# Kernel tuning notes

Measured on AMD Instinct MI355X. Metric: run time of the kernel, lower is better.

Reference implementation:

```python
import jax, jax.numpy as jnp
import numpy as np

N_ATOMS = 100000
N_EDGES = 800000
ATOM_DIM = 32
BOND_DIM = 16


def setup_inputs() -> dict:
    key = jax.random.key(0)
    k1, k2, k3, k4 = jax.random.split(key, 4)
    atom_features = jax.random.normal(k1, (N_ATOMS, ATOM_DIM), dtype=jnp.float32)
    bond_features = jax.random.normal(k2, (N_EDGES, BOND_DIM), dtype=jnp.float32)
    pair_indices = jax.random.randint(k3, (N_EDGES, 2), 0, N_ATOMS, dtype=jnp.int64 if jax.config.jax_enable_x64 else jnp.int32)
    # glorot-uniform-ish kernel
    limit = np.sqrt(6.0 / (BOND_DIM + ATOM_DIM * ATOM_DIM))
    kernel = jax.random.uniform(k4, (BOND_DIM, ATOM_DIM * ATOM_DIM), dtype=jnp.float32, minval=-limit, maxval=limit)
    bias = jnp.zeros((ATOM_DIM * ATOM_DIM,), dtype=jnp.float32)
    return {"atom_features": atom_features, "bond_features": bond_features,
            "pair_indices": pair_indices, "kernel": kernel, "bias": bias}


def reference(atom_features, bond_features, pair_indices, kernel, bias):
    atom_dim = atom_features.shape[-1]
    n_atoms = atom_features.shape[0]
    # bond-conditioned per-edge transform matrices: [E, atom_dim, atom_dim]
    bt = (bond_features @ kernel + bias).reshape(-1, atom_dim, atom_dim)
    # gather neighbor atom features: [E, atom_dim]
    neigh = atom_features[pair_indices[:, 1]]
    # per-edge small matmul: messages [E, atom_dim]
    messages = jnp.einsum('eij,ej->ei', bt, neigh)
    # scatter-add to destination atoms
    aggregated = jax.ops.segment_sum(messages, pair_indices[:, 0], num_segments=n_atoms)
    return aggregated
```

## Files before the change

### kernel.cpp

```cpp
#include <hip/hip_runtime.h>
#include <hip/hip_bf16.h>

typedef __attribute__((ext_vector_type(8))) short short8;
typedef __attribute__((ext_vector_type(4))) short s16x4;
typedef __attribute__((ext_vector_type(4))) float f32x4;

#define N_ATOMS 100000
#define N_EDGES 800000
#define N_TILES (N_EDGES/16)
#define WAVE_PAIRS 2048
#define N_CHUNKS ((N_ATOMS + 255) / 256)

#define WS_MSG     0ULL
#define WS_OFFS    51200000ULL
#define WS_COUNTS  51600016ULL
#define WS_EDATA   52000016ULL
#define WS_RANK    58400016ULL
#define WS_PART    61600016ULL
#define WS_NEED    61602064ULL

__device__ __forceinline__ short f2bf(float x) {
    __hip_bfloat16 h = __float2bfloat16(x);
    return __builtin_bit_cast(short, h);
}
__device__ __forceinline__ float bf2f(short b) {
    unsigned u = ((unsigned)(unsigned short)b) << 16;
    return __builtin_bit_cast(float, u);
}

__global__ __launch_bounds__(256) void zero_ints(int* __restrict__ p, int n) {
    int i = blockIdx.x * 256 + threadIdx.x;
    if (i < n) p[i] = 0;
}

__global__ __launch_bounds__(256) void rank_kernel(const int2* __restrict__ pair,
                                                   int* __restrict__ counts,
                                                   int* __restrict__ rank) {
    int e = blockIdx.x * 256 + threadIdx.x;
    if (e < N_EDGES) rank[e] = atomicAdd(&counts[pair[e].x], 1);
}

__global__ __launch_bounds__(256) void scan_part(const int* __restrict__ counts,
                                                 int* __restrict__ partials) {
    const int tid = threadIdx.x;
    const int i = blockIdx.x * 256 + tid;
    int v = (i < N_ATOMS) ? counts[i] : 0;
#pragma unroll
    for (int off = 1; off < 64; off <<= 1) v += __shfl_xor(v, off);
    __shared__ int ws4[4];
    const int lane = tid & 63, wv = tid >> 6;
    if (lane == 0) ws4[wv] = v;
    __syncthreads();
    if (tid == 0) partials[blockIdx.x] = ws4[0] + ws4[1] + ws4[2] + ws4[3];
}

__global__ __launch_bounds__(512) void scan_mid(int* __restrict__ partials) {
    const int tid = threadIdx.x;
    const int lane = tid & 63, wv = tid >> 6;
    int v = (tid < N_CHUNKS) ? partials[tid] : 0;
    int inc = v;
#pragma unroll
    for (int off = 1; off < 64; off <<= 1) {
        int u = __shfl_up(inc, off);
        if (lane >= off) inc += u;
    }
    __shared__ int ws8[8];
    if (lane == 63) ws8[wv] = inc;
    __syncthreads();
    int base = 0;
#pragma unroll
    for (int k = 0; k < 8; ++k) base += (k < wv) ? ws8[k] : 0;
    if (tid < N_CHUNKS) partials[tid] = base + inc - v;
}

__global__ __launch_bounds__(256) void scan_final(const int* __restrict__ counts,
                                                  const int* __restrict__ partials,
                                                  int* __restrict__ offsets) {
    const int tid = threadIdx.x;
    const int i = blockIdx.x * 256 + tid;
    const int lane = tid & 63, wv = tid >> 6;
    int c = (i < N_ATOMS) ? counts[i] : 0;
    int inc = c;
#pragma unroll
    for (int off = 1; off < 64; off <<= 1) {
        int u = __shfl_up(inc, off);
        if (lane >= off) inc += u;
    }
    __shared__ int ws4[4];
    if (lane == 63) ws4[wv] = inc;
    __syncthreads();
    int base = partials[blockIdx.x];
#pragma unroll
    for (int k = 0; k < 4; ++k) base += (k < wv) ? ws4[k] : 0;
    const int off = base + inc - c;
    if (i < N_ATOMS) offsets[i] = off;
    if (i == N_ATOMS - 1) offsets[N_ATOMS] = off + c;
}

__global__ __launch_bounds__(256) void edata_kernel(const int2* __restrict__ pair,
                                                    const int* __restrict__ offsets,
                                                    const int* __restrict__ rank,
                                                    int2* __restrict__ edata) {
    int e = blockIdx.x * 256 + threadIdx.x;
    if (e < N_EDGES) {
        int2 p = pair[e];
        int2 d;
        d.x = p.y;
        d.y = offsets[p.x] + rank[e];
        edata[e] = d;
    }
}

__global__ __launch_bounds__(256, 3)
void edge_msg_kernel(const float* __restrict__ atom,
                     const float* __restrict__ bond,
                     const float* __restrict__ kern,
                     const float* __restrict__ bias,
                     const int2*  __restrict__ edata,
                     short*       __restrict__ msg)
{
    __shared__ __align__(16) char smem[32768];
    short* klds = (short*)smem;
    float* blds = (float*)smem;

    const int tid = threadIdx.x;
    for (int x = tid; x < 16*2*512; x += 256) {
        const int t = x & 7;
        const int l = (x >> 3) & 63;
        const int m = (x >> 9) & 1;
        const int b = x >> 10;
        const int i = m*16 + (l & 15);
        const int j = ((l >> 4) << 3) + t;
        klds[x] = f2bf(kern[b*1024 + i*32 + j]);
    }
    __syncthreads();

    const int wave = tid >> 6;
    const int lane = tid & 63;
    const int er   = lane & 15;
    const int jg   = lane >> 4;
    const int wid  = blockIdx.x * 4 + wave;
    const int m    = wid & 1;
    const int pid  = wid >> 1;

    short8 afr[16];
#pragma unroll
    for (int b = 0; b < 16; ++b)
        afr[b] = *(const short8*)&klds[(b*2 + m)*512 + lane*8];

    short8 af16;
    {
        const float* bp = bias + (m*16 + er)*32 + jg*8;
        const f32x4 z0 = *(const f32x4*)bp;
        const f32x4 z1 = *(const f32x4*)(bp + 4);
        af16[0]=f2bf(z0[0]); af16[1]=f2bf(z0[1]); af16[2]=f2bf(z0[2]); af16[3]=f2bf(z0[3]);
        af16[4]=f2bf(z1[0]); af16[5]=f2bf(z1[1]); af16[6]=f2bf(z1[2]); af16[7]=f2bf(z1[3]);
    }
    __syncthreads();

    const int ibase = m*16 + jg*4;

    float* bwA = blds + (0*4 + wave)*320 + (lane >> 2)*20 + (lane & 3)*4;
    float* bwB = blds + (1*4 + wave)*320 + (lane >> 2)*20 + (lane & 3)*4;
    const float* brA = blds + (0*4 + wave)*320 + er*20;
    const float* brB = blds + (1*4 + wave)*320 + er*20;

    const int last = N_TILES - 1;

    const int tA = pid;
    const int tB = (pid + WAVE_PAIRS <= last) ? pid + WAVE_PAIRS : last;
    int2  e0 = edata[tA*16 + er];
    f32x4 bv0 = *(const f32x4*)(bond + tA*256 + lane*4);
    int2  e1 = edata[tB*16 + er];
    f32x4 bv1 = *(const f32x4*)(bond + tB*256 + lane*4);
    f32x4 n0 = *(const f32x4*)(atom + e0.x*32 + jg*8);
    f32x4 n1 = *(const f32x4*)(atom + e0.x*32 + jg*8 + 4);
    *(f32x4*)bwA = bv0;

    for (int t = pid; t < N_TILES; t += WAVE_PAIRS) {
        int tn2 = t + 2*WAVE_PAIRS; tn2 = (tn2 <= last) ? tn2 : last;
        const int2  e2  = edata[tn2*16 + er];
        const f32x4 bv2 = *(const f32x4*)(bond + tn2*256 + lane*4);

        const f32x4 n0n = *(const f32x4*)(atom + e1.x*32 + jg*8);
        const f32x4 n1n = *(const f32x4*)(atom + e1.x*32 + jg*8 + 4);

        const f32x4 q0 = *(const f32x4*)(brA + 0);
        const f32x4 q1 = *(const f32x4*)(brA + 4);
        const f32x4 q2 = *(const f32x4*)(brA + 8);
        const f32x4 q3 = *(const f32x4*)(brA + 12);

        short8 bfrag;
        bfrag[0] = f2bf(n0[0]); bfrag[1] = f2bf(n0[1]);
        bfrag[2] = f2bf(n0[2]); bfrag[3] = f2bf(n0[3]);
        bfrag[4] = f2bf(n1[0]); bfrag[5] = f2bf(n1[1]);
        bfrag[6] = f2bf(n1[2]); bfrag[7] = f2bf(n1[3]);

        float bb[16];
        bb[0]=q0[0];  bb[1]=q0[1];  bb[2]=q0[2];  bb[3]=q0[3];
        bb[4]=q1[0];  bb[5]=q1[1];  bb[6]=q1[2];  bb[7]=q1[3];
        bb[8]=q2[0];  bb[9]=q2[1];  bb[10]=q2[2]; bb[11]=q2[3];
        bb[12]=q3[0]; bb[13]=q3[1]; bb[14]=q3[2]; bb[15]=q3[3];

        f32x4 macc = {0.f,0.f,0.f,0.f};
        const f32x4 z = {0.f,0.f,0.f,0.f};
#pragma unroll
        for (int b = 0; b < 16; ++b) {
            f32x4 d = __builtin_amdgcn_mfma_f32_16x16x32_bf16(afr[b], bfrag, z, 0, 0, 0);
            macc[0] = fmaf(bb[b], d[0], macc[0]);
            macc[1] = fmaf(bb[b], d[1], macc[1]);
            macc[2] = fmaf(bb[b], d[2], macc[2]);
            macc[3] = fmaf(bb[b], d[3], macc[3]);
        }
        {
            f32x4 d = __builtin_amdgcn_mfma_f32_16x16x32_bf16(af16, bfrag, z, 0, 0, 0);
            macc[0] += d[0]; macc[1] += d[1]; macc[2] += d[2]; macc[3] += d[3];
        }

        *(f32x4*)bwB = bv1;

        s16x4 mv;
        mv[0] = f2bf(macc[0]); mv[1] = f2bf(macc[1]);
        mv[2] = f2bf(macc[2]); mv[3] = f2bf(macc[3]);
        *(s16x4*)&msg[(long long)e0.y*32 + ibase] = mv;

        e0 = e1; e1 = e2; bv1 = bv2; n0 = n0n; n1 = n1n;
        float* tw = bwA; bwA = bwB; bwB = tw;
        const float* tr = brA; brA = brB; brB = tr;
    }
}

__global__ __launch_bounds__(256) void gather_kernel(const short* __restrict__ msg,
                                                     const int* __restrict__ offsets,
                                                     float* __restrict__ out) {
    const int tid = threadIdx.x;
    const int a = blockIdx.x * 32 + (tid >> 3);
    const int sub = (tid & 7) * 4;
    if (a >= N_ATOMS) return;
    const int b0 = offsets[a], b1 = offsets[a + 1];
    f32x4 acc0 = {0.f, 0.f, 0.f, 0.f};
    f32x4 acc1 = {0.f, 0.f, 0.f, 0.f};
    int k = b0;
    for (; k + 1 < b1; k += 2) {
        s16x4 mv0 = *(const s16x4*)&msg[k*32 + sub];
        s16x4 mv1 = *(const s16x4*)&msg[(k+1)*32 + sub];
        acc0[0] += bf2f(mv0[0]); acc0[1] += bf2f(mv0[1]);
        acc0[2] += bf2f(mv0[2]); acc0[3] += bf2f(mv0[3]);
        acc1[0] += bf2f(mv1[0]); acc1[1] += bf2f(mv1[1]);
        acc1[2] += bf2f(mv1[2]); acc1[3] += bf2f(mv1[3]);
    }
    if (k < b1) {
        s16x4 mv0 = *(const s16x4*)&msg[k*32 + sub];
        acc0[0] += bf2f(mv0[0]); acc0[1] += bf2f(mv0[1]);
        acc0[2] += bf2f(mv0[2]); acc0[3] += bf2f(mv0[3]);
    }
    acc0[0] += acc1[0]; acc0[1] += acc1[1]; acc0[2] += acc1[2]; acc0[3] += acc1[3];
    *(f32x4*)&out[a*32 + sub] = acc0;
}

__global__ __launch_bounds__(256) void zero_out(f32x4* __restrict__ out) {
    int i = blockIdx.x * 256 + threadIdx.x;
    f32x4 z = {0.f, 0.f, 0.f, 0.f};
    out[i] = z;
}

__global__ __launch_bounds__(256, 4)
void edge_kernel_atomic(const float* __restrict__ atom, const float* __restrict__ bond,
                        const int2* __restrict__ pair, const float* __restrict__ kern,
                        const float* __restrict__ bias, float* __restrict__ out)
{
    __shared__ __align__(16) short alds[17*2*512];
    const int tid = threadIdx.x;
    for (int x = tid; x < 17*2*512; x += 256) {
        const int t = x & 7;
        const int l = (x >> 3) & 63;
        const int m = (x >> 9) & 1;
        const int b = x >> 10;
        const int i = m*16 + (l & 15);
        const int j = ((l >> 4) << 3) + t;
        const float v = (b < 16) ? kern[b*1024 + i*32 + j] : bias[i*32 + j];
        alds[x] = f2bf(v);
    }
    __syncthreads();
    const int wave = tid >> 6, lane = tid & 63;
    const int er = lane & 15, jg = lane >> 4;
    const int wid = blockIdx.x * 4 + wave;
    const int m = wid & 1, pid = wid >> 1;
    short8 afr[17];
#pragma unroll
    for (int b = 0; b < 17; ++b)
        afr[b] = *(const short8*)&alds[(b*2 + m)*512 + lane*8];
    const int ibase = m*16 + jg*4;
    for (int tile = pid; tile < N_TILES; tile += WAVE_PAIRS) {
        const int e = tile*16 + er;
        const int2 p = pair[e];
        const f32x4* arow = (const f32x4*)(atom + p.y * 32);
        const f32x4 n0 = arow[jg*2];
        const f32x4 n1 = arow[jg*2 + 1];
        short8 bfrag;
        bfrag[0] = f2bf(n0[0]); bfrag[1] = f2bf(n0[1]);
        bfrag[2] = f2bf(n0[2]); bfrag[3] = f2bf(n0[3]);
        bfrag[4] = f2bf(n1[0]); bfrag[5] = f2bf(n1[1]);
        bfrag[6] = f2bf(n1[2]); bfrag[7] = f2bf(n1[3]);
        const f32x4* brow = (const f32x4*)(bond + e * 16);
        const f32x4 q0 = brow[0], q1 = brow[1], q2 = brow[2], q3 = brow[3];
        float bb[17];
        bb[0]=q0[0];  bb[1]=q0[1];  bb[2]=q0[2];  bb[3]=q0[3];
        bb[4]=q1[0];  bb[5]=q1[1];  bb[6]=q1[2];  bb[7]=q1[3];
        bb[8]=q2[0];  bb[9]=q2[1];  bb[10]=q2[2]; bb[11]=q2[3];
        bb[12]=q3[0]; bb[13]=q3[1]; bb[14]=q3[2]; bb[15]=q3[3];
        bb[16]=1.0f;
        f32x4 macc = {0.f,0.f,0.f,0.f};
#pragma unroll
        for (int b = 0; b < 17; ++b) {
            f32x4 z = {0.f,0.f,0.f,0.f};
            f32x4 d = __builtin_amdgcn_mfma_f32_16x16x32_bf16(afr[b], bfrag, z, 0, 0, 0);
            macc[0] = fmaf(bb[b], d[0], macc[0]);
            macc[1] = fmaf(bb[b], d[1], macc[1]);
            macc[2] = fmaf(bb[b], d[2], macc[2]);
            macc[3] = fmaf(bb[b], d[3], macc[3]);
        }
        float* obase = out + p.x * 32 + ibase;
        atomicAdd(obase + 0, macc[0]);
        atomicAdd(obase + 1, macc[1]);
        atomicAdd(obase + 2, macc[2]);
        atomicAdd(obase + 3, macc[3]);
    }
}

extern "C" void kernel_launch(void* const* d_in, const int* in_sizes, int n_in,
                              void* d_out, int out_size, void* d_ws, size_t ws_size,
                              hipStream_t stream)
{
    (void)in_sizes; (void)n_in; (void)out_size;
    const float* atom = (const float*)d_in[0];
    const float* bond = (const float*)d_in[1];
    const int2*  pair = (const int2*)d_in[2];
    const float* kern = (const float*)d_in[3];
    const float* bias = (const float*)d_in[4];
    float* out = (float*)d_out;

    if (ws_size < WS_NEED) {
        zero_out<<<dim3(N_ATOMS*32/4/256), dim3(256), 0, stream>>>((f32x4*)out);
        edge_kernel_atomic<<<dim3(1024), dim3(256), 0, stream>>>(atom, bond, pair, kern, bias, out);
        return;
    }

    char* ws = (char*)d_ws;
    short* msg    = (short*)(ws + WS_MSG);
    int* offsets  = (int*)(ws + WS_OFFS);
    int* counts   = (int*)(ws + WS_COUNTS);
    int2* edata   = (int2*)(ws + WS_EDATA);
    int* rank     = (int*)(ws + WS_RANK);
    int* partials = (int*)(ws + WS_PART);

    const int eb = (N_EDGES + 255) / 256;
    zero_ints<<<dim3((N_ATOMS + 255)/256), dim3(256), 0, stream>>>(counts, N_ATOMS);
    rank_kernel<<<dim3(eb), dim3(256), 0, stream>>>(pair, counts, rank);
    scan_part<<<dim3(N_CHUNKS), dim3(256), 0, stream>>>(counts, partials);
    scan_mid<<<dim3(1), dim3(512), 0, stream>>>(partials);
    scan_final<<<dim3(N_CHUNKS), dim3(256), 0, stream>>>(counts, partials, offsets);
    edata_kernel<<<dim3(eb), dim3(256), 0, stream>>>(pair, offsets, rank, edata);
    edge_msg_kernel<<<dim3(1024), dim3(256), 0, stream>>>(atom, bond, kern, bias, edata, msg);
    gather_kernel<<<dim3((N_ATOMS + 31)/32), dim3(256), 0, stream>>>(msg, offsets, out);
}
```

Before: 117.2 us.

## Deepen edge-message prefetch pipeline and replace LDS bond staging with shuffles

Restructures the edge message kernel. The grid now has 1250 blocks, so each wave pair handles exactly 20 tiles, and the loop is a fixed 5x4 unrolled sequence. Edge data and bond rows are prefetched four tiles ahead and atom rows two tiles ahead, which raises the number of memory requests in flight. Bond values are now spread across lanes with wave shuffles instead of being staged through a double-buffered LDS area, which removes the LDS writes, reads and one barrier but adds 16 shuffles per tile and more live registers. The tile counts are hardcoded, so the kernel depends on N_TILES being exactly 20×2500.

```diff
diff --git a/kernel.cpp b/kernel.cpp
--- a/kernel.cpp
+++ b/kernel.cpp
@@ -8,8 +8,10 @@
 #define N_ATOMS 100000
 #define N_EDGES 800000
 #define N_TILES (N_EDGES/16)
-#define WAVE_PAIRS 2048
 #define N_CHUNKS ((N_ATOMS + 255) / 256)
+
+#define MSG_BLOCKS 1250
+#define S_TILES    2500
 
 #define WS_MSG     0ULL
 #define WS_OFFS    51200000ULL
@@ -119,9 +121,7 @@
                      const int2*  __restrict__ edata,
                      short*       __restrict__ msg)
 {
-    __shared__ __align__(16) char smem[32768];
-    short* klds = (short*)smem;
-    float* blds = (float*)smem;
+    __shared__ __align__(16) short klds[16*2*512];
 
     const int tid = threadIdx.x;
     for (int x = tid; x < 16*2*512; x += 256) {
@@ -156,78 +156,74 @@
         af16[0]=f2bf(z0[0]); af16[1]=f2bf(z0[1]); af16[2]=f2bf(z0[2]); af16[3]=f2bf(z0[3]);
         af16[4]=f2bf(z1[0]); af16[5]=f2bf(z1[1]); af16[6]=f2bf(z1[2]); af16[7]=f2bf(z1[3]);
     }
-    __syncthreads();
 
     const int ibase = m*16 + jg*4;
-
-    float* bwA = blds + (0*4 + wave)*320 + (lane >> 2)*20 + (lane & 3)*4;
-    float* bwB = blds + (1*4 + wave)*320 + (lane >> 2)*20 + (lane & 3)*4;
-    const float* brA = blds + (0*4 + wave)*320 + er*20;
-    const float* brB = blds + (1*4 + wave)*320 + er*20;
-
-    const int last = N_TILES - 1;
+    const int last  = N_TILES - 1;
 
     const int tA = pid;
-    const int tB = (pid + WAVE_PAIRS <= last) ? pid + WAVE_PAIRS : last;
-    int2  e0 = edata[tA*16 + er];
-    f32x4 bv0 = *(const f32x4*)(bond + tA*256 + lane*4);
-    int2  e1 = edata[tB*16 + er];
-    f32x4 bv1 = *(const f32x4*)(bond + tB*256 + lane*4);
-    f32x4 n0 = *(const f32x4*)(atom + e0.x*32 + jg*8);
-    f32x4 n1 = *(const f32x4*)(atom + e0.x*32 + jg*8 + 4);
-    *(f32x4*)bwA = bv0;
-
-    for (int t = pid; t < N_TILES; t += WAVE_PAIRS) {
-        int tn2 = t + 2*WAVE_PAIRS; tn2 = (tn2 <= last) ? tn2 : last;
-        const int2  e2  = edata[tn2*16 + er];
-        const f32x4 bv2 = *(const f32x4*)(bond + tn2*256 + lane*4);
-
-        const f32x4 n0n = *(const f32x4*)(atom + e1.x*32 + jg*8);
-        const f32x4 n1n = *(const f32x4*)(atom + e1.x*32 + jg*8 + 4);
-
-        const f32x4 q0 = *(const f32x4*)(brA + 0);
-        const f32x4 q1 = *(const f32x4*)(brA + 4);
-        const f32x4 q2 = *(const f32x4*)(brA + 8);
-        const f32x4 q3 = *(const f32x4*)(brA + 12);
-
-        short8 bfrag;
-        bfrag[0] = f2bf(n0[0]); bfrag[1] = f2bf(n0[1]);
-        bfrag[2] = f2bf(n0[2]); bfrag[3] = f2bf(n0[3]);
-        bfrag[4] = f2bf(n1[0]); bfrag[5] = f2bf(n1[1]);
-        bfrag[6] = f2bf(n1[2]); bfrag[7] = f2bf(n1[3]);
-
-        float bb[16];
-        bb[0]=q0[0];  bb[1]=q0[1];  bb[2]=q0[2];  bb[3]=q0[3];
-        bb[4]=q1[0];  bb[5]=q1[1];  bb[6]=q1[2];  bb[7]=q1[3];
-        bb[8]=q2[0];  bb[9]=q2[1];  bb[10]=q2[2]; bb[11]=q2[3];
-        bb[12]=q3[0]; bb[13]=q3[1]; bb[14]=q3[2]; bb[15]=q3[3];
-
-        f32x4 macc = {0.f,0.f,0.f,0.f};
-        const f32x4 z = {0.f,0.f,0.f,0.f};
-#pragma unroll
-        for (int b = 0; b < 16; ++b) {
-            f32x4 d = __builtin_amdgcn_mfma_f32_16x16x32_bf16(afr[b], bfrag, z, 0, 0, 0);
-            macc[0] = fmaf(bb[b], d[0], macc[0]);
-            macc[1] = fmaf(bb[b], d[1], macc[1]);
-            macc[2] = fmaf(bb[b], d[2], macc[2]);
-            macc[3] = fmaf(bb[b], d[3], macc[3]);
-        }
-        {
-            f32x4 d = __builtin_amdgcn_mfma_f32_16x16x32_bf16(af16, bfrag, z, 0, 0, 0);
-            macc[0] += d[0]; macc[1] += d[1]; macc[2] += d[2]; macc[3] += d[3];
-        }
-
-        *(f32x4*)bwB = bv1;
-
-        s16x4 mv;
-        mv[0] = f2bf(macc[0]); mv[1] = f2bf(macc[1]);
-        mv[2] = f2bf(macc[2]); mv[3] = f2bf(macc[3]);
-        *(s16x4*)&msg[(long long)e0.y*32 + ibase] = mv;
-
-        e0 = e1; e1 = e2; bv1 = bv2; n0 = n0n; n1 = n1n;
-        float* tw = bwA; bwA = bwB; bwB = tw;
-        const float* tr = brA; brA = brB; brB = tr;
-    }
+    const int tB = min(pid + 1*S_TILES, last);
+    const int tC = min(pid + 2*S_TILES, last);
+    const int tD = min(pid + 3*S_TILES, last);
+    int2  eA = edata[tA*16 + er];  f32x4 bvA = *(const f32x4*)(bond + tA*256 + lane*4);
+    int2  eB = edata[tB*16 + er];  f32x4 bvB = *(const f32x4*)(bond + tB*256 + lane*4);
+    int2  eC = edata[tC*16 + er];  f32x4 bvC = *(const f32x4*)(bond + tC*256 + lane*4);
+    int2  eD = edata[tD*16 + er];  f32x4 bvD = *(const f32x4*)(bond + tD*256 + lane*4);
+    f32x4 n0P = *(const f32x4*)(atom + eA.x*32 + jg*8);
+    f32x4 n1P = *(const f32x4*)(atom + eA.x*32 + jg*8 + 4);
+    f32x4 n0Q = *(const f32x4*)(atom + eB.x*32 + jg*8);
+    f32x4 n1Q = *(const f32x4*)(atom + eB.x*32 + jg*8 + 4);
+
+#define EMK_BODY(EC, BVC, N0, N1, EG, TK)                                          \
+    {                                                                              \
+        float bb[16];                                                              \
+        _Pragma("unroll")                                                          \
+        for (int q = 0; q < 4; ++q) {                                              \
+            const int sl2 = (er << 2) | q;                                         \
+            bb[q*4+0] = __shfl(BVC[0], sl2);                                       \
+            bb[q*4+1] = __shfl(BVC[1], sl2);                                       \
+            bb[q*4+2] = __shfl(BVC[2], sl2);                                       \
+            bb[q*4+3] = __shfl(BVC[3], sl2);                                       \
+        }                                                                          \
+        const int sl = EC.y;                                                       \
+        short8 bfrag;                                                              \
+        bfrag[0]=f2bf(N0[0]); bfrag[1]=f2bf(N0[1]);                                \
+        bfrag[2]=f2bf(N0[2]); bfrag[3]=f2bf(N0[3]);                                \
+        bfrag[4]=f2bf(N1[0]); bfrag[5]=f2bf(N1[1]);                                \
+        bfrag[6]=f2bf(N1[2]); bfrag[7]=f2bf(N1[3]);                                \
+        const int t4 = min((TK) + 4*S_TILES, last);                                \
+        EC  = edata[t4*16 + er];                                                   \
+        BVC = *(const f32x4*)(bond + t4*256 + lane*4);                             \
+        N0  = *(const f32x4*)(atom + EG.x*32 + jg*8);                              \
+        N1  = *(const f32x4*)(atom + EG.x*32 + jg*8 + 4);                          \
+        f32x4 macc = {0.f,0.f,0.f,0.f};                                            \
+        const f32x4 z = {0.f,0.f,0.f,0.f};                                         \
+        _Pragma("unroll")                                                          \
+        for (int b = 0; b < 16; ++b) {                                             \
+            f32x4 d = __builtin_amdgcn_mfma_f32_16x16x32_bf16(afr[b], bfrag, z, 0, 0, 0); \
+            macc[0] = fmaf(bb[b], d[0], macc[0]);                                  \
+            macc[1] = fmaf(bb[b], d[1], macc[1]);                                  \
+            macc[2] = fmaf(bb[b], d[2], macc[2]);                                  \
+            macc[3] = fmaf(bb[b], d[3], macc[3]);                                  \
+        }                                                                          \
+        {                                                                          \
+            f32x4 d = __builtin_amdgcn_mfma_f32_16x16x32_bf16(af16, bfrag, z, 0, 0, 0); \
+            macc[0] += d[0]; macc[1] += d[1]; macc[2] += d[2]; macc[3] += d[3];    \
+        }                                                                          \
+        s16x4 mv;                                                                  \
+        mv[0]=f2bf(macc[0]); mv[1]=f2bf(macc[1]);                                  \
+        mv[2]=f2bf(macc[2]); mv[3]=f2bf(macc[3]);                                  \
+        *(s16x4*)&msg[sl*32 + ibase] = mv;                                         \
+    }
+
+#pragma unroll 1
+    for (int o = 0; o < 5; ++o) {
+        const int tb = pid + o*4*S_TILES;
+        EMK_BODY(eA, bvA, n0P, n1P, eC, tb + 0*S_TILES);
+        EMK_BODY(eB, bvB, n0Q, n1Q, eD, tb + 1*S_TILES);
+        EMK_BODY(eC, bvC, n0P, n1P, eA, tb + 2*S_TILES);
+        EMK_BODY(eD, bvD, n0Q, n1Q, eB, tb + 3*S_TILES);
+    }
+#undef EMK_BODY
 }
 
 __global__ __launch_bounds__(256) void gather_kernel(const short* __restrict__ msg,
@@ -291,7 +287,7 @@
     for (int b = 0; b < 17; ++b)
         afr[b] = *(const short8*)&alds[(b*2 + m)*512 + lane*8];
     const int ibase = m*16 + jg*4;
-    for (int tile = pid; tile < N_TILES; tile += WAVE_PAIRS) {
+    for (int tile = pid; tile < N_TILES; tile += 2048) {
         const int e = tile*16 + er;
         const int2 p = pair[e];
         const f32x4* arow = (const f32x4*)(atom + p.y * 32);
@@ -361,6 +357,6 @@
     scan_mid<<<dim3(1), dim3(512), 0, stream>>>(partials);
     scan_final<<<dim3(N_CHUNKS), dim3(256), 0, stream>>>(counts, partials, offsets);
     edata_kernel<<<dim3(eb), dim3(256), 0, stream>>>(pair, offsets, rank, edata);
-    edge_msg_kernel<<<dim3(1024), dim3(256), 0, stream>>>(atom, bond, kern, bias, edata, msg);
+    edge_msg_kernel<<<dim3(MSG_BLOCKS), dim3(256), 0, stream>>>(atom, bond, kern, bias, edata, msg);
     gather_kernel<<<dim3((N_ATOMS + 31)/32), dim3(256), 0, stream>>>(msg, offsets, out);
 }
```

New measurement: 127.3 us. 1.09x slower.

## Compute both output halves per wave to halve redundant edge gathers

Applied to the files above, without the earlier changes.

Each wave now handles all 32 output rows of a 16-edge tile instead of splitting them across a wave pair. The goal is to load the neighbor atom rows, bond features and edge data once per tile rather than twice. One half of the kernel fragments stays in registers and the other half, plus the bias, is read from LDS every iteration; an empty asm offset stops the compiler from hoisting those LDS loads into registers. The bond staging buffer becomes single-buffered per wave, and the grid shrinks to 768 blocks. The trade-off is more LDS traffic and longer per-wave dependency chains in place of duplicated global loads.

```diff
diff --git a/kernel.cpp b/kernel.cpp
--- a/kernel.cpp
+++ b/kernel.cpp
@@ -8,8 +8,10 @@
 #define N_ATOMS 100000
 #define N_EDGES 800000
 #define N_TILES (N_EDGES/16)
-#define WAVE_PAIRS 2048
 #define N_CHUNKS ((N_ATOMS + 255) / 256)
+
+#define MSG_BLOCKS 768
+#define MSG_WAVES  (MSG_BLOCKS*4)
 
 #define WS_MSG     0ULL
 #define WS_OFFS    51200000ULL
@@ -119,19 +121,19 @@
                      const int2*  __restrict__ edata,
                      short*       __restrict__ msg)
 {
-    __shared__ __align__(16) char smem[32768];
-    short* klds = (short*)smem;
-    float* blds = (float*)smem;
-
-    const int tid = threadIdx.x;
-    for (int x = tid; x < 16*2*512; x += 256) {
+    __shared__ __align__(16) short klds[17*2*512];
+    __shared__ __align__(16) float blds[4*320];
+
+    const int tid = threadIdx.x;
+    for (int x = tid; x < 17*2*512; x += 256) {
         const int t = x & 7;
         const int l = (x >> 3) & 63;
         const int m = (x >> 9) & 1;
         const int b = x >> 10;
         const int i = m*16 + (l & 15);
         const int j = ((l >> 4) << 3) + t;
-        klds[x] = f2bf(kern[b*1024 + i*32 + j]);
+        const float v = (b < 16) ? kern[b*1024 + i*32 + j] : bias[i*32 + j];
+        klds[x] = f2bf(v);
     }
     __syncthreads();
 
@@ -139,94 +141,91 @@
     const int lane = tid & 63;
     const int er   = lane & 15;
     const int jg   = lane >> 4;
-    const int wid  = blockIdx.x * 4 + wave;
-    const int m    = wid & 1;
-    const int pid  = wid >> 1;
+    const int pid  = blockIdx.x * 4 + wave;
 
     short8 afr[16];
 #pragma unroll
     for (int b = 0; b < 16; ++b)
-        afr[b] = *(const short8*)&klds[(b*2 + m)*512 + lane*8];
-
-    short8 af16;
-    {
-        const float* bp = bias + (m*16 + er)*32 + jg*8;
-        const f32x4 z0 = *(const f32x4*)bp;
-        const f32x4 z1 = *(const f32x4*)(bp + 4);
-        af16[0]=f2bf(z0[0]); af16[1]=f2bf(z0[1]); af16[2]=f2bf(z0[2]); af16[3]=f2bf(z0[3]);
-        af16[4]=f2bf(z1[0]); af16[5]=f2bf(z1[1]); af16[6]=f2bf(z1[2]); af16[7]=f2bf(z1[3]);
-    }
-    __syncthreads();
-
-    const int ibase = m*16 + jg*4;
-
-    float* bwA = blds + (0*4 + wave)*320 + (lane >> 2)*20 + (lane & 3)*4;
-    float* bwB = blds + (1*4 + wave)*320 + (lane >> 2)*20 + (lane & 3)*4;
-    const float* brA = blds + (0*4 + wave)*320 + er*20;
-    const float* brB = blds + (1*4 + wave)*320 + er*20;
+        afr[b] = *(const short8*)&klds[b*1024 + lane*8];
+
+    const int ibase = jg*4;
+
+    float* bw = &blds[wave*320 + (lane >> 2)*20 + (lane & 3)*4];
+    const float* brd = &blds[wave*320 + er*20];
 
     const int last = N_TILES - 1;
 
-    const int tA = pid;
-    const int tB = (pid + WAVE_PAIRS <= last) ? pid + WAVE_PAIRS : last;
-    int2  e0 = edata[tA*16 + er];
-    f32x4 bv0 = *(const f32x4*)(bond + tA*256 + lane*4);
-    int2  e1 = edata[tB*16 + er];
-    f32x4 bv1 = *(const f32x4*)(bond + tB*256 + lane*4);
+    const int t1p = min(pid + MSG_WAVES, last);
+    int2  e0 = edata[pid*16 + er];
+    f32x4 bv0 = *(const f32x4*)(bond + pid*256 + lane*4);
+    int2  e1 = edata[t1p*16 + er];
+    f32x4 bv1 = *(const f32x4*)(bond + t1p*256 + lane*4);
+    *(f32x4*)bw = bv0;
     f32x4 n0 = *(const f32x4*)(atom + e0.x*32 + jg*8);
     f32x4 n1 = *(const f32x4*)(atom + e0.x*32 + jg*8 + 4);
-    *(f32x4*)bwA = bv0;
-
-    for (int t = pid; t < N_TILES; t += WAVE_PAIRS) {
-        int tn2 = t + 2*WAVE_PAIRS; tn2 = (tn2 <= last) ? tn2 : last;
-        const int2  e2  = edata[tn2*16 + er];
-        const f32x4 bv2 = *(const f32x4*)(bond + tn2*256 + lane*4);
+
+    for (int t = pid; t < N_TILES; t += MSG_WAVES) {
+        int koff = 0;
+        asm volatile("" : "+v"(koff));
 
         const f32x4 n0n = *(const f32x4*)(atom + e1.x*32 + jg*8);
         const f32x4 n1n = *(const f32x4*)(atom + e1.x*32 + jg*8 + 4);
 
-        const f32x4 q0 = *(const f32x4*)(brA + 0);
-        const f32x4 q1 = *(const f32x4*)(brA + 4);
-        const f32x4 q2 = *(const f32x4*)(brA + 8);
-        const f32x4 q3 = *(const f32x4*)(brA + 12);
-
         short8 bfrag;
-        bfrag[0] = f2bf(n0[0]); bfrag[1] = f2bf(n0[1]);
-        bfrag[2] = f2bf(n0[2]); bfrag[3] = f2bf(n0[3]);
-        bfrag[4] = f2bf(n1[0]); bfrag[5] = f2bf(n1[1]);
-        bfrag[6] = f2bf(n1[2]); bfrag[7] = f2bf(n1[3]);
-
-        float bb[16];
-        bb[0]=q0[0];  bb[1]=q0[1];  bb[2]=q0[2];  bb[3]=q0[3];
-        bb[4]=q1[0];  bb[5]=q1[1];  bb[6]=q1[2];  bb[7]=q1[3];
-        bb[8]=q2[0];  bb[9]=q2[1];  bb[10]=q2[2]; bb[11]=q2[3];
-        bb[12]=q3[0]; bb[13]=q3[1]; bb[14]=q3[2]; bb[15]=q3[3];
-
-        f32x4 macc = {0.f,0.f,0.f,0.f};
+        bfrag[0]=f2bf(n0[0]); bfrag[1]=f2bf(n0[1]);
+        bfrag[2]=f2bf(n0[2]); bfrag[3]=f2bf(n0[3]);
+        bfrag[4]=f2bf(n1[0]); bfrag[5]=f2bf(n1[1]);
+        bfrag[6]=f2bf(n1[2]); bfrag[7]=f2bf(n1[3]);
+
+        f32x4 macc0 = {0.f,0.f,0.f,0.f};
+        f32x4 macc1 = {0.f,0.f,0.f,0.f};
         const f32x4 z = {0.f,0.f,0.f,0.f};
-#pragma unroll
-        for (int b = 0; b < 16; ++b) {
-            f32x4 d = __builtin_amdgcn_mfma_f32_16x16x32_bf16(afr[b], bfrag, z, 0, 0, 0);
-            macc[0] = fmaf(bb[b], d[0], macc[0]);
-            macc[1] = fmaf(bb[b], d[1], macc[1]);
-            macc[2] = fmaf(bb[b], d[2], macc[2]);
-            macc[3] = fmaf(bb[b], d[3], macc[3]);
+
+#pragma unroll
+        for (int g = 0; g < 4; ++g) {
+            const f32x4 q = *(const f32x4*)(brd + g*4);
+#pragma unroll
+            for (int c = 0; c < 4; ++c) {
+                const int b = g*4 + c;
+                const short8 a1 = *(const short8*)&klds[b*1024 + 512 + lane*8 + koff];
+                const f32x4 d0 = __builtin_amdgcn_mfma_f32_16x16x32_bf16(afr[b], bfrag, z, 0, 0, 0);
+                const f32x4 d1 = __builtin_amdgcn_mfma_f32_16x16x32_bf16(a1,     bfrag, z, 0, 0, 0);
+                macc0[0] = fmaf(q[c], d0[0], macc0[0]);
+                macc0[1] = fmaf(q[c], d0[1], macc0[1]);
+                macc0[2] = fmaf(q[c], d0[2], macc0[2]);
+                macc0[3] = fmaf(q[c], d0[3], macc0[3]);
+                macc1[0] = fmaf(q[c], d1[0], macc1[0]);
+                macc1[1] = fmaf(q[c], d1[1], macc1[1]);
+                macc1[2] = fmaf(q[c], d1[2], macc1[2]);
+                macc1[3] = fmaf(q[c], d1[3], macc1[3]);
+            }
         }
         {
-            f32x4 d = __builtin_amdgcn_mfma_f32_16x16x32_bf16(af16, bfrag, z, 0, 0, 0);
-            macc[0] += d[0]; macc[1] += d[1]; macc[2] += d[2]; macc[3] += d[3];
+            const short8 ab0 = *(const short8*)&klds[16*1024 +       lane*8 + koff];
+            const short8 ab1 = *(const short8*)&klds[16*1024 + 512 + lane*8 + koff];
+            const f32x4 d0 = __builtin_amdgcn_mfma_f32_16x16x32_bf16(ab0, bfrag, z, 0, 0, 0);
+            const f32x4 d1 = __builtin_amdgcn_mfma_f32_16x16x32_bf16(ab1, bfrag, z, 0, 0, 0);
+            macc0[0] += d0[0]; macc0[1] += d0[1]; macc0[2] += d0[2]; macc0[3] += d0[3];
+            macc1[0] += d1[0]; macc1[1] += d1[1]; macc1[2] += d1[2]; macc1[3] += d1[3];
         }
 
-        *(f32x4*)bwB = bv1;
-
-        s16x4 mv;
-        mv[0] = f2bf(macc[0]); mv[1] = f2bf(macc[1]);
-        mv[2] = f2bf(macc[2]); mv[3] = f2bf(macc[3]);
-        *(s16x4*)&msg[(long long)e0.y*32 + ibase] = mv;
-
-        e0 = e1; e1 = e2; bv1 = bv2; n0 = n0n; n1 = n1n;
-        float* tw = bwA; bwA = bwB; bwB = tw;
-        const float* tr = brA; brA = brB; brB = tr;
+        const int t2 = min(t + 2*MSG_WAVES, last);
+        const int2  e2  = edata[t2*16 + er];
+        const f32x4 bv2 = *(const f32x4*)(bond + t2*256 + lane*4);
+
+        *(f32x4*)bw = bv1;
+
+        const int sl = e0.y;
+        s16x4 mv0, mv1;
+        mv0[0]=f2bf(macc0[0]); mv0[1]=f2bf(macc0[1]);
+        mv0[2]=f2bf(macc0[2]); mv0[3]=f2bf(macc0[3]);
+        mv1[0]=f2bf(macc1[0]); mv1[1]=f2bf(macc1[1]);
+        mv1[2]=f2bf(macc1[2]); mv1[3]=f2bf(macc1[3]);
+        *(s16x4*)&msg[sl*32 + ibase]      = mv0;
+        *(s16x4*)&msg[sl*32 + 16 + ibase] = mv1;
+
+        e0 = e1; e1 = e2; bv1 = bv2;
+        n0 = n0n; n1 = n1n;
     }
 }
 
@@ -291,7 +290,7 @@
     for (int b = 0; b < 17; ++b)
         afr[b] = *(const short8*)&alds[(b*2 + m)*512 + lane*8];
     const int ibase = m*16 + jg*4;
-    for (int tile = pid; tile < N_TILES; tile += WAVE_PAIRS) {
+    for (int tile = pid; tile < N_TILES; tile += 2048) {
         const int e = tile*16 + er;
         const int2 p = pair[e];
         const f32x4* arow = (const f32x4*)(atom + p.y * 32);
@@ -361,6 +360,6 @@
     scan_mid<<<dim3(1), dim3(512), 0, stream>>>(partials);
     scan_final<<<dim3(N_CHUNKS), dim3(256), 0, stream>>>(counts, partials, offsets);
     edata_kernel<<<dim3(eb), dim3(256), 0, stream>>>(pair, offsets, rank, edata);
-    edge_msg_kernel<<<dim3(1024), dim3(256), 0, stream>>>(atom, bond, kern, bias, edata, msg);
+    edge_msg_kernel<<<dim3(MSG_BLOCKS), dim3(256), 0, stream>>>(atom, bond, kern, bias, edata, msg);
     gather_kernel<<<dim3((N_ATOMS + 31)/32), dim3(256), 0, stream>>>(msg, offsets, out);
 }
```

Result: faster. 112.3 us (-4.1%).
